# Kernel tuning notes

Hardware: AMD Instinct MI355X
Metric: run time of the kernel (lower is better)

The kernel has to match this reference:

```python
import jax, jax.numpy as jnp
import numpy as np

D_MODEL = 1024
D_CTRL = 1024
N_HEADS = 16
TOPK = 4
TEMPERATURE = 1.0
LN_EPS = 1e-5


def layer_norm(x, g, b):
    m = jnp.mean(x, axis=-1, keepdims=True)
    v = jnp.mean(jnp.square(x - m), axis=-1, keepdims=True)
    return (x - m) * jax.lax.rsqrt(v + LN_EPS) * g + b


def setup_inputs() -> dict:
    key = jax.random.key(0)
    ks = jax.random.split(key, 8)
    B, S = 8, 2048
    s = 0.02
    return {
        "x": jax.random.normal(ks[0], (B, S, D_MODEL), dtype=jnp.float32),
        "state": jnp.zeros((B, D_CTRL), dtype=jnp.float32),
        # pool LayerNorm
        "pool_g": jnp.ones((D_MODEL,), jnp.float32),
        "pool_b": jnp.zeros((D_MODEL,), jnp.float32),
        # inp_proj
        "inp_w": jax.random.normal(ks[1], (D_MODEL, D_CTRL), jnp.float32) * s,
        "inp_b": jnp.zeros((D_CTRL,), jnp.float32),
        # W_z, W_h
        "wz_w": jax.random.normal(ks[2], (D_CTRL, D_CTRL), jnp.float32) * s,
        "wz_b": jnp.zeros((D_CTRL,), jnp.float32),
        "wh_w": jax.random.normal(ks[3], (D_CTRL, D_CTRL), jnp.float32) * s,
        "wh_b": jnp.zeros((D_CTRL,), jnp.float32),
        # ln_h
        "lnh_g": jnp.ones((D_CTRL,), jnp.float32),
        "lnh_b": jnp.zeros((D_CTRL,), jnp.float32),
        # router: LayerNorm(d_model+d_ctrl) -> Linear -> GELU -> Linear
        "rln_g": jnp.ones((D_MODEL + D_CTRL,), jnp.float32),
        "rln_b": jnp.zeros((D_MODEL + D_CTRL,), jnp.float32),
        "r_w1": jax.random.normal(ks[4], (D_MODEL + D_CTRL, D_CTRL), jnp.float32) * s,
        "r_b1": jnp.zeros((D_CTRL,), jnp.float32),
        "r_w2": jax.random.normal(ks[5], (D_CTRL, N_HEADS), jnp.float32) * s,
        "r_b2": jnp.zeros((N_HEADS,), jnp.float32),
    }


def reference(x, state, pool_g, pool_b, inp_w, inp_b, wz_w, wz_b, wh_w, wh_b,
              lnh_g, lnh_b, rln_g, rln_b, r_w1, r_b1, r_w2, r_b2):
    B, S, D = x.shape
    # pool: LayerNorm over tokens then mean over sequence -> [B, d_model]
    g = jnp.mean(layer_norm(x, pool_g, pool_b), axis=1)
    x_ctrl = g @ inp_w + inp_b  # [B, d_ctrl]
    z = jax.nn.sigmoid(x_ctrl @ wz_w + wz_b)
    h_cand = jnp.tanh(x_ctrl @ wh_w + wh_b)
    h_new = (1.0 - z) * state + z * h_cand
    h_new = layer_norm(h_new, lnh_g, lnh_b)  # [B, d_ctrl]
    # token-conditioned router on concat([X, h_tok])
    h_tok = jnp.broadcast_to(h_new[:, None, :], (B, S, D_CTRL))
    cat = jnp.concatenate([x, h_tok], axis=-1)  # [B, S, d_model+d_ctrl]
    hid = jax.nn.gelu(layer_norm(cat, rln_g, rln_b) @ r_w1 + r_b1, approximate=False)
    logits = hid @ r_w2 + r_b2  # [B, S, H]
    alpha = jax.nn.softmax(logits / TEMPERATURE, axis=-1)
    # top-k mask + renorm
    _, topi = jax.lax.top_k(alpha, TOPK)  # [B, S, k]
    mask = jnp.sum(jax.nn.one_hot(topi, N_HEADS, dtype=alpha.dtype), axis=-2)  # [B, S, H]
    masked = alpha * mask
    denom = jnp.maximum(jnp.sum(masked, axis=-1, keepdims=True), 1e-12)
    alpha = masked / denom
    entropy = -jnp.mean(jnp.sum(alpha * jnp.log(jnp.maximum(alpha, 1e-12)), axis=-1))
    return (alpha, h_new, entropy)
```

## Files before the change

### kernel.cpp

```cpp
#include <hip/hip_runtime.h>
#include <hip/hip_bf16.h>
#include <math.h>

typedef unsigned short u16;
typedef __attribute__((ext_vector_type(8))) short bf16x8;
typedef __attribute__((ext_vector_type(4))) float f32x4;
typedef __attribute__((ext_vector_type(4))) unsigned short u16x4;

#define B_ 8
#define S_ 2048
#define T_ 16384
#define D_ 1024
#define H_ 16
#define EPS_ 1e-5f

__device__ __forceinline__ u16 f2bf(float f) {
    __hip_bfloat16 h = __float2bfloat16(f);
    union { __hip_bfloat16 h; u16 u; } cv; cv.h = h; return cv.u;
}
__device__ __forceinline__ float bf2f(u16 u) {
    union { u16 u; __hip_bfloat16 h; } cv; cv.u = u; return __bfloat162float(cv.h);
}

__global__ __launch_bounds__(256) void k0a(const float* __restrict__ rw1,
        const float* __restrict__ rlng, const float* __restrict__ rlnb,
        u16* __restrict__ whiT, u16* __restrict__ wloT,
        float* __restrict__ c1part, float* __restrict__ c2part) {
    int nb = blockIdx.x, kb = blockIdx.y;
    int t = threadIdx.x;
    int nl = t & 63, kq = t >> 6;
    int n0 = nb * 64, k0 = kb * 64;
    __shared__ float ld[64][65];
    __shared__ float red[2][4][64];
    float a1 = 0.f, a2 = 0.f;
    #pragma unroll
    for (int r = 0; r < 16; ++r) {
        int kl = r * 4 + kq;
        int k = k0 + kl, n = n0 + nl;
        float w0 = rw1[(size_t)k * 1024 + n];
        ld[kl][nl] = w0;
        a1 += rlng[k] * w0;
        a2 += rlnb[k] * w0;
    }
    red[0][kq][nl] = a1;
    red[1][kq][nl] = a2;
    __syncthreads();
    if (t < 64) {
        c1part[(size_t)kb * 1024 + n0 + t] = red[0][0][t] + red[0][1][t] + red[0][2][t] + red[0][3][t];
        c2part[(size_t)kb * 1024 + n0 + t] = red[1][0][t] + red[1][1][t] + red[1][2][t] + red[1][3][t];
    }
    if (kb < 16) {
        #pragma unroll
        for (int r = 0; r < 16; ++r) {
            int nl2 = r * 4 + kq;
            int k = k0 + nl, n = n0 + nl2;
            float w0 = ld[nl][nl2] * rlng[k];
            u16 hi = f2bf(w0);
            float lo = w0 - bf2f(hi);
            whiT[(size_t)n * 1024 + k] = hi;
            wloT[(size_t)n * 1024 + k] = f2bf(lo);
        }
    }
}

__global__ __launch_bounds__(256) void k1(const float* __restrict__ x,
        u16* __restrict__ xhi, u16* __restrict__ xlo,
        float* __restrict__ sx, float* __restrict__ sxx, float* __restrict__ gpart) {
    int blk = blockIdx.x;
    int b = blk >> 5, chunk = blk & 31;
    int tid = threadIdx.x, w = tid >> 6, lane = tid & 63;
    __shared__ float lacc[4][1024];
    float acc[4][4];
    #pragma unroll
    for (int j = 0; j < 4; ++j)
        #pragma unroll
        for (int c = 0; c < 4; ++c) acc[j][c] = 0.f;

    for (int i = 0; i < 16; ++i) {
        int s = chunk * 64 + i * 4 + w;
        size_t tok = (size_t)b * S_ + s;
        size_t base = tok * D_;
        float4 v[4];
        float sum = 0.f, ssq = 0.f;
        #pragma unroll
        for (int j = 0; j < 4; ++j) {
            v[j] = *(const float4*)&x[base + j * 256 + lane * 4];
            sum += v[j].x + v[j].y + v[j].z + v[j].w;
            ssq += v[j].x * v[j].x + v[j].y * v[j].y + v[j].z * v[j].z + v[j].w * v[j].w;
        }
        #pragma unroll
        for (int m = 1; m < 64; m <<= 1) { sum += __shfl_xor(sum, m); ssq += __shfl_xor(ssq, m); }
        float mean = sum * (1.f / 1024.f);
        float var = ssq * (1.f / 1024.f) - mean * mean;
        float rstd = rsqrtf(var + EPS_);
        if (lane == 0) { sx[tok] = sum; sxx[tok] = ssq; }
        #pragma unroll
        for (int j = 0; j < 4; ++j) {
            float xs[4] = { v[j].x, v[j].y, v[j].z, v[j].w };
            u16 hs[4], ls[4];
            #pragma unroll
            for (int c = 0; c < 4; ++c) {
                acc[j][c] += (xs[c] - mean) * rstd;
                u16 h = f2bf(xs[c]);
                hs[c] = h;
                ls[c] = f2bf(xs[c] - bf2f(h));
            }
            size_t o = base + j * 256 + lane * 4;
            *(u16x4*)&xhi[o] = (u16x4){ hs[0], hs[1], hs[2], hs[3] };
            *(u16x4*)&xlo[o] = (u16x4){ ls[0], ls[1], ls[2], ls[3] };
        }
    }
    #pragma unroll
    for (int j = 0; j < 4; ++j)
        #pragma unroll
        for (int c = 0; c < 4; ++c) lacc[w][j * 256 + lane * 4 + c] = acc[j][c];
    __syncthreads();
    for (int q = 0; q < 4; ++q) {
        int n = q * 256 + tid;
        gpart[((size_t)b * 32 + chunk) * 1024 + n] =
            lacc[0][n] + lacc[1][n] + lacc[2][n] + lacc[3][n];
    }
}

__global__ __launch_bounds__(256) void kgemv_g(const float* __restrict__ gpart,
        const float* __restrict__ pg, const float* __restrict__ pb,
        const float* __restrict__ W, float* __restrict__ part) {
    int t = threadIdx.x;
    int n = blockIdx.x * 256 + t;
    int k0 = blockIdx.y * 32;
    __shared__ float sg[8][32];
    {
        int b = t >> 5, k = t & 31;
        float s = 0.f;
        #pragma unroll 8
        for (int p = 0; p < 32; ++p) s += gpart[((size_t)b * 32 + p) * 1024 + k0 + k];
        sg[b][k] = s * (1.f / 2048.f) * pg[k0 + k] + pb[k0 + k];
    }
    __syncthreads();
    float acc[8] = {};
    #pragma unroll
    for (int k = 0; k < 32; ++k) {
        float wv = W[(size_t)(k0 + k) * 1024 + n];
        #pragma unroll
        for (int b = 0; b < 8; ++b) acc[b] += sg[b][k] * wv;
    }
    #pragma unroll
    for (int b = 0; b < 8; ++b)
        part[((size_t)blockIdx.y * 8 + b) * 1024 + n] = acc[b];
}

__global__ __launch_bounds__(256) void kgemv_split(const float* __restrict__ in,
        const float* __restrict__ W, const float* __restrict__ scale,
        float* __restrict__ part) {
    int t = threadIdx.x;
    int n = blockIdx.x * 256 + t;
    int k0 = blockIdx.y * 32;
    __shared__ float sg[8][32];
    {
        int b = t >> 5, k = t & 31;
        float v = in[b * 1024 + k0 + k];
        if (scale) v *= scale[k0 + k];
        sg[b][k] = v;
    }
    __syncthreads();
    float acc[8] = {};
    #pragma unroll
    for (int k = 0; k < 32; ++k) {
        float wv = W[(size_t)(k0 + k) * 1024 + n];
        #pragma unroll
        for (int b = 0; b < 8; ++b) acc[b] += sg[b][k] * wv;
    }
    #pragma unroll
    for (int b = 0; b < 8; ++b)
        part[((size_t)blockIdx.y * 8 + b) * 1024 + n] = acc[b];
}

__global__ __launch_bounds__(256) void kgemv2_f(const float* __restrict__ partIn,
        const float* __restrict__ bias,
        const float* __restrict__ Wz, const float* __restrict__ Wh,
        float* __restrict__ zpart, float* __restrict__ hpart) {
    int t = threadIdx.x;
    int n = blockIdx.x * 256 + t;
    int k0 = blockIdx.y * 32;
    __shared__ float sg[8][32];
    {
        int b = t >> 5, k = t & 31;
        float s = bias[k0 + k];
        #pragma unroll 8
        for (int p = 0; p < 32; ++p) s += partIn[((size_t)p * 8 + b) * 1024 + k0 + k];
        sg[b][k] = s;
    }
    __syncthreads();
    float az[8] = {}, ah[8] = {};
    #pragma unroll
    for (int k = 0; k < 32; ++k) {
        size_t o = (size_t)(k0 + k) * 1024 + n;
        float wz = Wz[o];
        float wh = Wh[o];
        #pragma unroll
        for (int b = 0; b < 8; ++b) { az[b] += sg[b][k] * wz; ah[b] += sg[b][k] * wh; }
    }
    #pragma unroll
    for (int b = 0; b < 8; ++b) {
        size_t o = ((size_t)blockIdx.y * 8 + b) * 1024 + n;
        zpart[o] = az[b];
        hpart[o] = ah[b];
    }
}

__global__ __launch_bounds__(256) void k3b_red_ln(const float* __restrict__ zpart,
        const float* __restrict__ hpart, const float* __restrict__ bz,
        const float* __restrict__ bh, const float* __restrict__ state,
        const float* __restrict__ lg, const float* __restrict__ lb,
        float* __restrict__ hnew, float* __restrict__ outh,
        float* __restrict__ shb, float* __restrict__ shhb) {
    int b = blockIdx.x, tid = threadIdx.x;
    int w = tid >> 6, lane = tid & 63;
    __shared__ float rbuf[4][2];
    float hp[4];
    float sum = 0.f, ssq = 0.f;
    #pragma unroll
    for (int q = 0; q < 4; ++q) {
        int n = q * 256 + tid;
        float az = bz[n], ah = bh[n];
        #pragma unroll 8
        for (int p = 0; p < 32; ++p) {
            size_t o = ((size_t)p * 8 + b) * 1024 + n;
            az += zpart[o];
            ah += hpart[o];
        }
        float z = 1.f / (1.f + expf(-az));
        float hc = tanhf(ah);
        float v = (1.f - z) * state[(size_t)b * 1024 + n] + z * hc;
        hp[q] = v; sum += v; ssq += v * v;
    }
    #pragma unroll
    for (int m = 1; m < 64; m <<= 1) { sum += __shfl_xor(sum, m); ssq += __shfl_xor(ssq, m); }
    if (lane == 0) { rbuf[w][0] = sum; rbuf[w][1] = ssq; }
    __syncthreads();
    sum = rbuf[0][0] + rbuf[1][0] + rbuf[2][0] + rbuf[3][0];
    ssq = rbuf[0][1] + rbuf[1][1] + rbuf[2][1] + rbuf[3][1];
    float mean = sum * (1.f / 1024.f);
    float var = ssq * (1.f / 1024.f) - mean * mean;
    float rstd = rsqrtf(var + EPS_);
    float s2 = 0.f, q2 = 0.f;
    #pragma unroll
    for (int q = 0; q < 4; ++q) {
        int n = q * 256 + tid;
        float h = (hp[q] - mean) * rstd * lg[n] + lb[n];
        hnew[(size_t)b * 1024 + n] = h;
        outh[(size_t)b * 1024 + n] = h;
        s2 += h; q2 += h * h;
    }
    #pragma unroll
    for (int m = 1; m < 64; m <<= 1) { s2 += __shfl_xor(s2, m); q2 += __shfl_xor(q2, m); }
    __syncthreads();
    if (lane == 0) { rbuf[w][0] = s2; rbuf[w][1] = q2; }
    __syncthreads();
    if (tid == 0) {
        shb[b] = rbuf[0][0] + rbuf[1][0] + rbuf[2][0] + rbuf[3][0];
        shhb[b] = rbuf[0][1] + rbuf[1][1] + rbuf[2][1] + rbuf[3][1];
    }
}

__global__ __launch_bounds__(256) void kprep(const float* __restrict__ vpartIn,
        const float* __restrict__ c1part, const float* __restrict__ c2part,
        const float* __restrict__ rb1,
        const float* __restrict__ sx, const float* __restrict__ sxx,
        const float* __restrict__ shb, const float* __restrict__ shhb,
        float* __restrict__ vmat, float* __restrict__ c1, float* __restrict__ dvec,
        float* __restrict__ pt, float* __restrict__ qt) {
    int blk = blockIdx.x, tid = threadIdx.x;
    if (blk < 32) {
        int i = blk * 256 + tid;
        int b = i >> 10, n = i & 1023;
        float s = 0.f;
        #pragma unroll 8
        for (int p = 0; p < 32; ++p) s += vpartIn[((size_t)p * 8 + b) * 1024 + n];
        vmat[i] = s;
    } else if (blk < 36) {
        int n = (blk - 32) * 256 + tid;
        float s1 = 0.f, s2 = 0.f;
        for (int p = 0; p < 32; ++p) { s1 += c1part[p * 1024 + n]; s2 += c2part[p * 1024 + n]; }
        c1[n] = s1;
        dvec[n] = s2 + rb1[n];
    } else {
        int t = (blk - 36) * 256 + tid;
        int b = t >> 11;
        float m = (sx[t] + shb[b]) * (1.f / 2048.f);
        float var = (sxx[t] + shhb[b]) * (1.f / 2048.f) - m * m;
        float rstd = rsqrtf(var + EPS_);
        pt[t] = rstd;
        qt[t] = -m * rstd;
    }
}

__device__ __forceinline__ void gl16(const void* g, void* l) {
    __builtin_amdgcn_global_load_lds((const __attribute__((address_space(1))) void*)g,
                                     (__attribute__((address_space(3))) void*)l, 16, 0, 0);
}

__global__ __launch_bounds__(256, 1) void k5_gemm(
        const u16* __restrict__ xhi, const u16* __restrict__ xlo,
        const u16* __restrict__ whiT, const u16* __restrict__ wloT,
        const float* __restrict__ pt, const float* __restrict__ qt,
        const float* __restrict__ vmat, const float* __restrict__ c1,
        const float* __restrict__ dvec, const float* __restrict__ rw2,
        float* __restrict__ lpart) {
    __shared__ unsigned char smem[66048];
    u16* sAh = (u16*)smem;
    u16* sAl = sAh + 128 * 64;
    u16* sBh = sAl + 128 * 64;
    u16* sBl = sBh + 128 * 64;
    float* shid = (float*)smem;

    int bid = blockIdx.x;
    int x8 = bid & 7, j = bid >> 3;
    int mb = x8 * 16 + (j >> 3);
    int nb = j & 7;
    int tid = threadIdx.x;
    int lane = tid & 63, wid = tid >> 6;
    int wm = wid >> 1, wn = wid & 1;
    int l16 = lane & 15, lq = lane >> 4;

    f32x4 acc[4][4] = {};

    size_t aBase = (size_t)mb * 128 * 1024;
    size_t bBase = (size_t)nb * 128 * 1024;

    for (int kb = 0; kb < 16; ++kb) {
        __syncthreads();
        #pragma unroll
        for (int i = 0; i < 4; ++i) {
            int chunk = tid + 256 * i;
            int row = chunk >> 3, c8 = chunk & 7;
            int s8 = c8 ^ (row & 7);
            size_t go = (size_t)row * 1024 + (size_t)kb * 64 + s8 * 8;
            int lo = chunk * 16;
            gl16(xhi + aBase + go, (char*)sAh + lo);
            gl16(xlo + aBase + go, (char*)sAl + lo);
            gl16(whiT + bBase + go, (char*)sBh + lo);
            gl16(wloT + bBase + go, (char*)sBl + lo);
        }
        asm volatile("s_waitcnt vmcnt(0)" ::: "memory");
        __syncthreads();
        #pragma unroll
        for (int kk = 0; kk < 2; ++kk) {
            bf16x8 ah[4], al[4], bh[4], bl[4];
            int sl = ((kk * 4 + lq) ^ (l16 & 7)) * 8;
            #pragma unroll
            for (int f = 0; f < 4; ++f) {
                int ar = wm * 64 + f * 16 + l16;
                int br = wn * 64 + f * 16 + l16;
                ah[f] = *(const bf16x8*)&sAh[ar * 64 + sl];
                al[f] = *(const bf16x8*)&sAl[ar * 64 + sl];
                bh[f] = *(const bf16x8*)&sBh[br * 64 + sl];
                bl[f] = *(const bf16x8*)&sBl[br * 64 + sl];
            }
            #pragma unroll
            for (int mf = 0; mf < 4; ++mf)
                #pragma unroll
                for (int nf = 0; nf < 4; ++nf) {
                    acc[mf][nf] = __builtin_amdgcn_mfma_f32_16x16x32_bf16(ah[mf], bh[nf], acc[mf][nf], 0, 0, 0);
                    acc[mf][nf] = __builtin_amdgcn_mfma_f32_16x16x32_bf16(ah[mf], bl[nf], acc[mf][nf], 0, 0, 0);
                    acc[mf][nf] = __builtin_amdgcn_mfma_f32_16x16x32_bf16(al[mf], bh[nf], acc[mf][nf], 0, 0, 0);
                }
        }
    }
    __syncthreads();

    int token0 = mb * 128;
    int bidx = token0 >> 11;
    const float* vrow = vmat + (size_t)bidx * 1024;
    float vn[4], c1n[4], dn[4];
    #pragma unroll
    for (int nf = 0; nf < 4; ++nf) {
        int n = nb * 128 + wn * 64 + nf * 16 + l16;
        vn[nf] = vrow[n]; c1n[nf] = c1[n]; dn[nf] = dvec[n];
    }
    #pragma unroll
    for (int mf = 0; mf < 4; ++mf) {
        #pragma unroll
        for (int r = 0; r < 4; ++r) {
            int rowl = wm * 64 + mf * 16 + lq * 4 + r;
            float p = pt[token0 + rowl];
            float q = qt[token0 + rowl];
            #pragma unroll
            for (int nf = 0; nf < 4; ++nf) {
                int coll = wn * 64 + nf * 16 + l16;
                float pre = p * (acc[mf][nf][r] + vn[nf]) + q * c1n[nf] + dn[nf];
                float hid = 0.5f * pre * (1.f + erff(pre * 0.70710678118f));
                shid[rowl * 129 + coll] = hid;
            }
        }
    }
    __syncthreads();

    int r2 = tid >> 1, half = tid & 1;
    const float* w2b = rw2 + (size_t)nb * 128 * 16 + half * 8;
    float a8[8];
    #pragma unroll
    for (int h = 0; h < 8; ++h) a8[h] = 0.f;
    #pragma unroll 8
    for (int j2 = 0; j2 < 128; ++j2) {
        float hv = shid[r2 * 129 + j2];
        float4 w0 = *(const float4*)(w2b + (size_t)j2 * 16);
        float4 w1 = *(const float4*)(w2b + (size_t)j2 * 16 + 4);
        a8[0] += hv * w0.x; a8[1] += hv * w0.y; a8[2] += hv * w0.z; a8[3] += hv * w0.w;
        a8[4] += hv * w1.x; a8[5] += hv * w1.y; a8[6] += hv * w1.z; a8[7] += hv * w1.w;
    }
    float* lp = lpart + ((size_t)nb * T_ + token0 + r2) * 16 + half * 8;
    #pragma unroll
    for (int h = 0; h < 8; ++h) lp[h] = a8[h];
}

__global__ __launch_bounds__(256) void k6(const float* __restrict__ lpart,
        const float* __restrict__ rb2, float* __restrict__ alpha_out,
        float* __restrict__ entpart) {
    int blk = blockIdx.x;
    int tid = threadIdx.x;
    int token = blk * 16 + (tid >> 4);
    int h = tid & 15;
    float lg = rb2[h];
    #pragma unroll
    for (int p = 0; p < 8; ++p) lg += lpart[((size_t)p * T_ + token) * 16 + h];

    float mx = lg;
    #pragma unroll
    for (int m = 1; m < 16; m <<= 1) mx = fmaxf(mx, __shfl_xor(mx, m));
    float e = expf(lg - mx);
    float sum = e;
    #pragma unroll
    for (int m = 1; m < 16; m <<= 1) sum += __shfl_xor(sum, m);
    float a0 = e / sum;

    float work = lg;
    bool sel = false;
    #pragma unroll
    for (int it = 0; it < 4; ++it) {
        float bv = work; int bi = h;
        #pragma unroll
        for (int m = 1; m < 16; m <<= 1) {
            float ov = __shfl_xor(bv, m); int oi = __shfl_xor(bi, m);
            if (ov > bv || (ov == bv && oi < bi)) { bv = ov; bi = oi; }
        }
        if (h == bi) { sel = true; work = -1e30f; }
    }
    float am = sel ? a0 : 0.f;
    float den = am;
    #pragma unroll
    for (int m = 1; m < 16; m <<= 1) den += __shfl_xor(den, m);
    den = fmaxf(den, 1e-12f);
    float a = am / den;
    alpha_out[(size_t)token * 16 + h] = a;

    float term = a * logf(fmaxf(a, 1e-12f));
    #pragma unroll
    for (int m = 1; m < 64; m <<= 1) term += __shfl_xor(term, m);
    __shared__ float tw[4];
    if ((tid & 63) == 0) tw[tid >> 6] = term;
    __syncthreads();
    if (tid == 0) entpart[blk] = tw[0] + tw[1] + tw[2] + tw[3];
}

__global__ __launch_bounds__(256) void k7(const float* __restrict__ entpart,
        float* __restrict__ out_ent) {
    int tid = threadIdx.x;
    float s = 0.f;
    for (int i = tid; i < 1024; i += 256) s += entpart[i];
    #pragma unroll
    for (int m = 1; m < 64; m <<= 1) s += __shfl_xor(s, m);
    __shared__ float tw[4];
    if ((tid & 63) == 0) tw[tid >> 6] = s;
    __syncthreads();
    if (tid == 0) out_ent[0] = -(tw[0] + tw[1] + tw[2] + tw[3]) * (1.f / (float)T_);
}

extern "C" void kernel_launch(void* const* d_in, const int* in_sizes, int n_in,
                              void* d_out, int out_size, void* d_ws, size_t ws_size,
                              hipStream_t stream) {
    const float* x     = (const float*)d_in[0];
    const float* state = (const float*)d_in[1];
    const float* pg    = (const float*)d_in[2];
    const float* pbv   = (const float*)d_in[3];
    const float* inpw  = (const float*)d_in[4];
    const float* inpb  = (const float*)d_in[5];
    const float* wzw   = (const float*)d_in[6];
    const float* wzb   = (const float*)d_in[7];
    const float* whw   = (const float*)d_in[8];
    const float* whb   = (const float*)d_in[9];
    const float* lnhg  = (const float*)d_in[10];
    const float* lnhb  = (const float*)d_in[11];
    const float* rlng  = (const float*)d_in[12];
    const float* rlnb  = (const float*)d_in[13];
    const float* rw1   = (const float*)d_in[14];
    const float* rb1   = (const float*)d_in[15];
    const float* rw2   = (const float*)d_in[16];
    const float* rb2   = (const float*)d_in[17];
    float* out = (float*)d_out;
    (void)in_sizes; (void)n_in; (void)out_size; (void)ws_size;

    char* base = (char*)d_ws;
    size_t off = 0;
    auto alloc = [&](size_t bytes) -> char* {
        char* p = base + off;
        off = (off + bytes + 255) & ~(size_t)255;
        return p;
    };
    u16*   xhi    = (u16*)alloc((size_t)T_ * D_ * 2);
    u16*   xlo    = (u16*)alloc((size_t)T_ * D_ * 2);
    u16*   whiT   = (u16*)alloc((size_t)D_ * D_ * 2);
    u16*   wloT   = (u16*)alloc((size_t)D_ * D_ * 2);
    float* c1part = (float*)alloc(32 * 1024 * 4);
    float* c2part = (float*)alloc(32 * 1024 * 4);
    float* c1     = (float*)alloc(1024 * 4);
    float* dvec   = (float*)alloc(1024 * 4);
    float* sx     = (float*)alloc((size_t)T_ * 4);
    float* sxx    = (float*)alloc((size_t)T_ * 4);
    float* ptv    = (float*)alloc((size_t)T_ * 4);
    float* qtv    = (float*)alloc((size_t)T_ * 4);
    float* gpart  = (float*)alloc((size_t)8 * 32 * 1024 * 4);
    float* hnew   = (float*)alloc(8 * 1024 * 4);
    float* vmat   = (float*)alloc(8 * 1024 * 4);
    float* shb    = (float*)alloc(256);
    float* shhb   = (float*)alloc(256);
    float* lpart  = (float*)alloc((size_t)8 * T_ * H_ * 4);
    float* entpart= (float*)alloc(1024 * 4);
    float* partA  = (float*)alloc((size_t)32 * 8 * 1024 * 4);
    float* partB  = (float*)alloc((size_t)32 * 8 * 1024 * 4);
    float* partC  = (float*)alloc((size_t)32 * 8 * 1024 * 4);

    k0a<<<dim3(16, 32), 256, 0, stream>>>(rw1, rlng, rlnb, whiT, wloT, c1part, c2part);
    k1<<<256, 256, 0, stream>>>(x, xhi, xlo, sx, sxx, gpart);
    kgemv_g<<<dim3(4, 32), 256, 0, stream>>>(gpart, pg, pbv, inpw, partA);
    kgemv2_f<<<dim3(4, 32), 256, 0, stream>>>(partA, inpb, wzw, whw, partB, partC);
    k3b_red_ln<<<8, 256, 0, stream>>>(partB, partC, wzb, whb, state, lnhg, lnhb,
                                      hnew, out + (size_t)T_ * H_, shb, shhb);
    kgemv_split<<<dim3(4, 32), 256, 0, stream>>>(hnew, rw1 + (size_t)1024 * 1024,
                                                 rlng + 1024, partA);
    kprep<<<100, 256, 0, stream>>>(partA, c1part, c2part, rb1, sx, sxx, shb, shhb,
                                   vmat, c1, dvec, ptv, qtv);
    k5_gemm<<<1024, 256, 0, stream>>>(xhi, xlo, whiT, wloT, ptv, qtv, vmat,
                                      c1, dvec, rw2, lpart);
    k6<<<1024, 256, 0, stream>>>(lpart, rb2, out, entpart);
    k7<<<1, 256, 0, stream>>>(entpart, out + (size_t)T_ * H_ + (size_t)B_ * D_);
}
```

Before: 203.0 us.

## Merge prep kernels and read GEMM B tiles directly from global memory

Merges the weight-prep and x-split kernels into one launch, folds the c1/dvec reduction into the first GEMV kernel, and moves the token-stat computation into the hnew GEMV kernel, splitting the vmat reduction into its own small kernel. In the main GEMM, the B operand (whiT/wloT) is no longer staged in LDS and is loaded per fragment straight from global memory. LDS use drops by half, and the epilogue processes the hidden tile in two 64-row halves. The aim is fewer launches and higher occupancy, at the cost of uncached, redundant global loads for B, which may be slower.

New measurement: 270.2 us. 1.33x slower.

```diff
diff --git a/kernel.cpp b/kernel.cpp
--- a/kernel.cpp
+++ b/kernel.cpp
@@ -22,157 +22,142 @@
     union { u16 u; __hip_bfloat16 h; } cv; cv.u = u; return __bfloat162float(cv.h);
 }
 
-__global__ __launch_bounds__(256) void k0a(const float* __restrict__ rw1,
-        const float* __restrict__ rlng, const float* __restrict__ rlnb,
-        u16* __restrict__ whiT, u16* __restrict__ wloT,
+__global__ __launch_bounds__(256) void k01(const float* __restrict__ x,
+        u16* __restrict__ xhi, u16* __restrict__ xlo,
+        float* __restrict__ sx, float* __restrict__ sxx, float* __restrict__ gpart,
+        const float* __restrict__ rw1, const float* __restrict__ rlng,
+        const float* __restrict__ rlnb, u16* __restrict__ whiT, u16* __restrict__ wloT,
         float* __restrict__ c1part, float* __restrict__ c2part) {
-    int nb = blockIdx.x, kb = blockIdx.y;
-    int t = threadIdx.x;
-    int nl = t & 63, kq = t >> 6;
-    int n0 = nb * 64, k0 = kb * 64;
+    __shared__ float lacc[4][1024];
     __shared__ float ld[64][65];
     __shared__ float red[2][4][64];
-    float a1 = 0.f, a2 = 0.f;
-    #pragma unroll
-    for (int r = 0; r < 16; ++r) {
-        int kl = r * 4 + kq;
-        int k = k0 + kl, n = n0 + nl;
-        float w0 = rw1[(size_t)k * 1024 + n];
-        ld[kl][nl] = w0;
-        a1 += rlng[k] * w0;
-        a2 += rlnb[k] * w0;
-    }
-    red[0][kq][nl] = a1;
-    red[1][kq][nl] = a2;
-    __syncthreads();
-    if (t < 64) {
-        c1part[(size_t)kb * 1024 + n0 + t] = red[0][0][t] + red[0][1][t] + red[0][2][t] + red[0][3][t];
-        c2part[(size_t)kb * 1024 + n0 + t] = red[1][0][t] + red[1][1][t] + red[1][2][t] + red[1][3][t];
-    }
-    if (kb < 16) {
+    int blk = blockIdx.x;
+    int tid = threadIdx.x;
+    if (blk < 256) {
+        int b = blk >> 5, chunk = blk & 31;
+        int w = tid >> 6, lane = tid & 63;
+        float acc[4][4];
+        #pragma unroll
+        for (int j = 0; j < 4; ++j)
+            #pragma unroll
+            for (int c = 0; c < 4; ++c) acc[j][c] = 0.f;
+        for (int i = 0; i < 16; ++i) {
+            int s = chunk * 64 + i * 4 + w;
+            size_t tok = (size_t)b * S_ + s;
+            size_t base = tok * D_;
+            float4 v[4];
+            float sum = 0.f, ssq = 0.f;
+            #pragma unroll
+            for (int j = 0; j < 4; ++j) {
+                v[j] = *(const float4*)&x[base + j * 256 + lane * 4];
+                sum += v[j].x + v[j].y + v[j].z + v[j].w;
+                ssq += v[j].x * v[j].x + v[j].y * v[j].y + v[j].z * v[j].z + v[j].w * v[j].w;
+            }
+            #pragma unroll
+            for (int m = 1; m < 64; m <<= 1) { sum += __shfl_xor(sum, m); ssq += __shfl_xor(ssq, m); }
+            float mean = sum * (1.f / 1024.f);
+            float var = ssq * (1.f / 1024.f) - mean * mean;
+            float rstd = rsqrtf(var + EPS_);
+            if (lane == 0) { sx[tok] = sum; sxx[tok] = ssq; }
+            #pragma unroll
+            for (int j = 0; j < 4; ++j) {
+                float xs[4] = { v[j].x, v[j].y, v[j].z, v[j].w };
+                u16 hs[4], ls[4];
+                #pragma unroll
+                for (int c = 0; c < 4; ++c) {
+                    acc[j][c] += (xs[c] - mean) * rstd;
+                    u16 h = f2bf(xs[c]);
+                    hs[c] = h;
+                    ls[c] = f2bf(xs[c] - bf2f(h));
+                }
+                size_t o = base + j * 256 + lane * 4;
+                *(u16x4*)&xhi[o] = (u16x4){ hs[0], hs[1], hs[2], hs[3] };
+                *(u16x4*)&xlo[o] = (u16x4){ ls[0], ls[1], ls[2], ls[3] };
+            }
+        }
+        #pragma unroll
+        for (int j = 0; j < 4; ++j)
+            #pragma unroll
+            for (int c = 0; c < 4; ++c) lacc[w][j * 256 + lane * 4 + c] = acc[j][c];
+        __syncthreads();
+        for (int q = 0; q < 4; ++q) {
+            int n = q * 256 + tid;
+            gpart[((size_t)b * 32 + chunk) * 1024 + n] =
+                lacc[0][n] + lacc[1][n] + lacc[2][n] + lacc[3][n];
+        }
+    } else {
+        int idx = blk - 256;
+        int nb = idx & 15, kb = idx >> 4;
+        int nl = tid & 63, kq = tid >> 6;
+        int n0 = nb * 64, k0 = kb * 64;
+        float a1 = 0.f, a2 = 0.f;
         #pragma unroll
         for (int r = 0; r < 16; ++r) {
-            int nl2 = r * 4 + kq;
-            int k = k0 + nl, n = n0 + nl2;
-            float w0 = ld[nl][nl2] * rlng[k];
-            u16 hi = f2bf(w0);
-            float lo = w0 - bf2f(hi);
-            whiT[(size_t)n * 1024 + k] = hi;
-            wloT[(size_t)n * 1024 + k] = f2bf(lo);
-        }
-    }
-}
-
-__global__ __launch_bounds__(256) void k1(const float* __restrict__ x,
-        u16* __restrict__ xhi, u16* __restrict__ xlo,
-        float* __restrict__ sx, float* __restrict__ sxx, float* __restrict__ gpart) {
-    int blk = blockIdx.x;
-    int b = blk >> 5, chunk = blk & 31;
-    int tid = threadIdx.x, w = tid >> 6, lane = tid & 63;
-    __shared__ float lacc[4][1024];
-    float acc[4][4];
-    #pragma unroll
-    for (int j = 0; j < 4; ++j)
-        #pragma unroll
-        for (int c = 0; c < 4; ++c) acc[j][c] = 0.f;
-
-    for (int i = 0; i < 16; ++i) {
-        int s = chunk * 64 + i * 4 + w;
-        size_t tok = (size_t)b * S_ + s;
-        size_t base = tok * D_;
-        float4 v[4];
-        float sum = 0.f, ssq = 0.f;
-        #pragma unroll
-        for (int j = 0; j < 4; ++j) {
-            v[j] = *(const float4*)&x[base + j * 256 + lane * 4];
-            sum += v[j].x + v[j].y + v[j].z + v[j].w;
-            ssq += v[j].x * v[j].x + v[j].y * v[j].y + v[j].z * v[j].z + v[j].w * v[j].w;
-        }
-        #pragma unroll
-        for (int m = 1; m < 64; m <<= 1) { sum += __shfl_xor(sum, m); ssq += __shfl_xor(ssq, m); }
-        float mean = sum * (1.f / 1024.f);
-        float var = ssq * (1.f / 1024.f) - mean * mean;
-        float rstd = rsqrtf(var + EPS_);
-        if (lane == 0) { sx[tok] = sum; sxx[tok] = ssq; }
-        #pragma unroll
-        for (int j = 0; j < 4; ++j) {
-            float xs[4] = { v[j].x, v[j].y, v[j].z, v[j].w };
-            u16 hs[4], ls[4];
-            #pragma unroll
-            for (int c = 0; c < 4; ++c) {
-                acc[j][c] += (xs[c] - mean) * rstd;
-                u16 h = f2bf(xs[c]);
-                hs[c] = h;
-                ls[c] = f2bf(xs[c] - bf2f(h));
+            int kl = r * 4 + kq;
+            int k = k0 + kl, n = n0 + nl;
+            float w0 = rw1[(size_t)k * 1024 + n];
+            ld[kl][nl] = w0;
+            a1 += rlng[k] * w0;
+            a2 += rlnb[k] * w0;
+        }
+        red[0][kq][nl] = a1;
+        red[1][kq][nl] = a2;
+        __syncthreads();
+        if (tid < 64) {
+            c1part[(size_t)kb * 1024 + n0 + tid] = red[0][0][tid] + red[0][1][tid] + red[0][2][tid] + red[0][3][tid];
+            c2part[(size_t)kb * 1024 + n0 + tid] = red[1][0][tid] + red[1][1][tid] + red[1][2][tid] + red[1][3][tid];
+        }
+        if (kb < 16) {
+            #pragma unroll
+            for (int r = 0; r < 16; ++r) {
+                int nl2 = r * 4 + kq;
+                int k = k0 + nl, n = n0 + nl2;
+                float w0 = ld[nl][nl2] * rlng[k];
+                u16 hi = f2bf(w0);
+                float lo = w0 - bf2f(hi);
+                whiT[(size_t)n * 1024 + k] = hi;
+                wloT[(size_t)n * 1024 + k] = f2bf(lo);
             }
-            size_t o = base + j * 256 + lane * 4;
-            *(u16x4*)&xhi[o] = (u16x4){ hs[0], hs[1], hs[2], hs[3] };
-            *(u16x4*)&xlo[o] = (u16x4){ ls[0], ls[1], ls[2], ls[3] };
-        }
-    }
-    #pragma unroll
-    for (int j = 0; j < 4; ++j)
-        #pragma unroll
-        for (int c = 0; c < 4; ++c) lacc[w][j * 256 + lane * 4 + c] = acc[j][c];
-    __syncthreads();
-    for (int q = 0; q < 4; ++q) {
-        int n = q * 256 + tid;
-        gpart[((size_t)b * 32 + chunk) * 1024 + n] =
-            lacc[0][n] + lacc[1][n] + lacc[2][n] + lacc[3][n];
-    }
-}
-
-__global__ __launch_bounds__(256) void kgemv_g(const float* __restrict__ gpart,
+        }
+    }
+}
+
+__global__ __launch_bounds__(256) void kB(const float* __restrict__ gpart,
         const float* __restrict__ pg, const float* __restrict__ pb,
-        const float* __restrict__ W, float* __restrict__ part) {
-    int t = threadIdx.x;
-    int n = blockIdx.x * 256 + t;
-    int k0 = blockIdx.y * 32;
-    __shared__ float sg[8][32];
-    {
-        int b = t >> 5, k = t & 31;
-        float s = 0.f;
-        #pragma unroll 8
-        for (int p = 0; p < 32; ++p) s += gpart[((size_t)b * 32 + p) * 1024 + k0 + k];
-        sg[b][k] = s * (1.f / 2048.f) * pg[k0 + k] + pb[k0 + k];
-    }
-    __syncthreads();
-    float acc[8] = {};
-    #pragma unroll
-    for (int k = 0; k < 32; ++k) {
-        float wv = W[(size_t)(k0 + k) * 1024 + n];
-        #pragma unroll
-        for (int b = 0; b < 8; ++b) acc[b] += sg[b][k] * wv;
-    }
-    #pragma unroll
-    for (int b = 0; b < 8; ++b)
-        part[((size_t)blockIdx.y * 8 + b) * 1024 + n] = acc[b];
-}
-
-__global__ __launch_bounds__(256) void kgemv_split(const float* __restrict__ in,
-        const float* __restrict__ W, const float* __restrict__ scale,
-        float* __restrict__ part) {
-    int t = threadIdx.x;
-    int n = blockIdx.x * 256 + t;
-    int k0 = blockIdx.y * 32;
-    __shared__ float sg[8][32];
-    {
-        int b = t >> 5, k = t & 31;
-        float v = in[b * 1024 + k0 + k];
-        if (scale) v *= scale[k0 + k];
-        sg[b][k] = v;
-    }
-    __syncthreads();
-    float acc[8] = {};
-    #pragma unroll
-    for (int k = 0; k < 32; ++k) {
-        float wv = W[(size_t)(k0 + k) * 1024 + n];
-        #pragma unroll
-        for (int b = 0; b < 8; ++b) acc[b] += sg[b][k] * wv;
-    }
-    #pragma unroll
-    for (int b = 0; b < 8; ++b)
-        part[((size_t)blockIdx.y * 8 + b) * 1024 + n] = acc[b];
+        const float* __restrict__ W, float* __restrict__ part,
+        const float* __restrict__ c1part, const float* __restrict__ c2part,
+        const float* __restrict__ rb1, float* __restrict__ c1, float* __restrict__ dvec) {
+    int blk = blockIdx.x, t = threadIdx.x;
+    if (blk < 128) {
+        int nBlk = blk & 3, ks = blk >> 2;
+        int n = nBlk * 256 + t;
+        int k0 = ks * 32;
+        __shared__ float sg[8][32];
+        {
+            int b = t >> 5, k = t & 31;
+            float s = 0.f;
+            #pragma unroll 8
+            for (int p = 0; p < 32; ++p) s += gpart[((size_t)b * 32 + p) * 1024 + k0 + k];
+            sg[b][k] = s * (1.f / 2048.f) * pg[k0 + k] + pb[k0 + k];
+        }
+        __syncthreads();
+        float acc[8] = {};
+        #pragma unroll
+        for (int k = 0; k < 32; ++k) {
+            float wv = W[(size_t)(k0 + k) * 1024 + n];
+            #pragma unroll
+            for (int b = 0; b < 8; ++b) acc[b] += sg[b][k] * wv;
+        }
+        #pragma unroll
+        for (int b = 0; b < 8; ++b)
+            part[((size_t)ks * 8 + b) * 1024 + n] = acc[b];
+    } else {
+        int n = (blk - 128) * 256 + t;
+        float s1 = 0.f, s2 = 0.f;
+        for (int p = 0; p < 32; ++p) { s1 += c1part[p * 1024 + n]; s2 += c2part[p * 1024 + n]; }
+        c1[n] = s1;
+        dvec[n] = s2 + rb1[n];
+    }
 }
 
 __global__ __launch_bounds__(256) void kgemv2_f(const float* __restrict__ partIn,
@@ -263,36 +248,52 @@
     }
 }
 
-__global__ __launch_bounds__(256) void kprep(const float* __restrict__ vpartIn,
-        const float* __restrict__ c1part, const float* __restrict__ c2part,
-        const float* __restrict__ rb1,
+__global__ __launch_bounds__(256) void kE(const float* __restrict__ in,
+        const float* __restrict__ W, const float* __restrict__ scale,
+        float* __restrict__ part,
         const float* __restrict__ sx, const float* __restrict__ sxx,
         const float* __restrict__ shb, const float* __restrict__ shhb,
-        float* __restrict__ vmat, float* __restrict__ c1, float* __restrict__ dvec,
         float* __restrict__ pt, float* __restrict__ qt) {
-    int blk = blockIdx.x, tid = threadIdx.x;
-    if (blk < 32) {
-        int i = blk * 256 + tid;
-        int b = i >> 10, n = i & 1023;
-        float s = 0.f;
-        #pragma unroll 8
-        for (int p = 0; p < 32; ++p) s += vpartIn[((size_t)p * 8 + b) * 1024 + n];
-        vmat[i] = s;
-    } else if (blk < 36) {
-        int n = (blk - 32) * 256 + tid;
-        float s1 = 0.f, s2 = 0.f;
-        for (int p = 0; p < 32; ++p) { s1 += c1part[p * 1024 + n]; s2 += c2part[p * 1024 + n]; }
-        c1[n] = s1;
-        dvec[n] = s2 + rb1[n];
+    int blk = blockIdx.x, t = threadIdx.x;
+    if (blk < 128) {
+        int nBlk = blk & 3, ks = blk >> 2;
+        int n = nBlk * 256 + t;
+        int k0 = ks * 32;
+        __shared__ float sg[8][32];
+        {
+            int b = t >> 5, k = t & 31;
+            sg[b][k] = in[b * 1024 + k0 + k] * scale[k0 + k];
+        }
+        __syncthreads();
+        float acc[8] = {};
+        #pragma unroll
+        for (int k = 0; k < 32; ++k) {
+            float wv = W[(size_t)(k0 + k) * 1024 + n];
+            #pragma unroll
+            for (int b = 0; b < 8; ++b) acc[b] += sg[b][k] * wv;
+        }
+        #pragma unroll
+        for (int b = 0; b < 8; ++b)
+            part[((size_t)ks * 8 + b) * 1024 + n] = acc[b];
     } else {
-        int t = (blk - 36) * 256 + tid;
-        int b = t >> 11;
-        float m = (sx[t] + shb[b]) * (1.f / 2048.f);
-        float var = (sxx[t] + shhb[b]) * (1.f / 2048.f) - m * m;
+        int tok = (blk - 128) * 256 + t;
+        int b = tok >> 11;
+        float m = (sx[tok] + shb[b]) * (1.f / 2048.f);
+        float var = (sxx[tok] + shhb[b]) * (1.f / 2048.f) - m * m;
         float rstd = rsqrtf(var + EPS_);
-        pt[t] = rstd;
-        qt[t] = -m * rstd;
-    }
+        pt[tok] = rstd;
+        qt[tok] = -m * rstd;
+    }
+}
+
+__global__ __launch_bounds__(256) void kF(const float* __restrict__ part,
+        float* __restrict__ vmat) {
+    int i = blockIdx.x * 256 + threadIdx.x;
+    int b = i >> 10, n = i & 1023;
+    float s = 0.f;
+    #pragma unroll 8
+    for (int p = 0; p < 32; ++p) s += part[((size_t)p * 8 + b) * 1024 + n];
+    vmat[i] = s;
 }
 
 __device__ __forceinline__ void gl16(const void* g, void* l) {
@@ -307,11 +308,9 @@
         const float* __restrict__ vmat, const float* __restrict__ c1,
         const float* __restrict__ dvec, const float* __restrict__ rw2,
         float* __restrict__ lpart) {
-    __shared__ unsigned char smem[66048];
+    __shared__ unsigned char smem[33024];
     u16* sAh = (u16*)smem;
     u16* sAl = sAh + 128 * 64;
-    u16* sBh = sAl + 128 * 64;
-    u16* sBl = sBh + 128 * 64;
     float* shid = (float*)smem;
 
     int bid = blockIdx.x;
@@ -336,11 +335,8 @@
             int row = chunk >> 3, c8 = chunk & 7;
             int s8 = c8 ^ (row & 7);
             size_t go = (size_t)row * 1024 + (size_t)kb * 64 + s8 * 8;
-            int lo = chunk * 16;
-            gl16(xhi + aBase + go, (char*)sAh + lo);
-            gl16(xlo + aBase + go, (char*)sAl + lo);
-            gl16(whiT + bBase + go, (char*)sBh + lo);
-            gl16(wloT + bBase + go, (char*)sBl + lo);
+            gl16(xhi + aBase + go, (char*)sAh + chunk * 16);
+            gl16(xlo + aBase + go, (char*)sAl + chunk * 16);
         }
         asm volatile("s_waitcnt vmcnt(0)" ::: "memory");
         __syncthreads();
@@ -352,10 +348,11 @@
             for (int f = 0; f < 4; ++f) {
                 int ar = wm * 64 + f * 16 + l16;
                 int br = wn * 64 + f * 16 + l16;
+                size_t gb = bBase + (size_t)br * 1024 + (size_t)kb * 64 + kk * 32 + lq * 8;
                 ah[f] = *(const bf16x8*)&sAh[ar * 64 + sl];
                 al[f] = *(const bf16x8*)&sAl[ar * 64 + sl];
-                bh[f] = *(const bf16x8*)&sBh[br * 64 + sl];
-                bl[f] = *(const bf16x8*)&sBl[br * 64 + sl];
+                bh[f] = *(const bf16x8*)&whiT[gb];
+                bl[f] = *(const bf16x8*)&wloT[gb];
             }
             #pragma unroll
             for (int mf = 0; mf < 4; ++mf)
@@ -367,7 +364,6 @@
                 }
         }
     }
-    __syncthreads();
 
     int token0 = mb * 128;
     int bidx = token0 >> 11;
@@ -379,39 +375,39 @@
         vn[nf] = vrow[n]; c1n[nf] = c1[n]; dn[nf] = dvec[n];
     }
     #pragma unroll
-    for (int mf = 0; mf < 4; ++mf) {
-        #pragma unroll
-        for (int r = 0; r < 4; ++r) {
-            int rowl = wm * 64 + mf * 16 + lq * 4 + r;
-            float p = pt[token0 + rowl];
-            float q = qt[token0 + rowl];
-            #pragma unroll
-            for (int nf = 0; nf < 4; ++nf) {
-                int coll = wn * 64 + nf * 16 + l16;
-                float pre = p * (acc[mf][nf][r] + vn[nf]) + q * c1n[nf] + dn[nf];
-                float hid = 0.5f * pre * (1.f + erff(pre * 0.70710678118f));
-                shid[rowl * 129 + coll] = hid;
+    for (int c = 0; c < 2; ++c) {
+        __syncthreads();
+        if (wm == c) {
+            #pragma unroll
+            for (int mf = 0; mf < 4; ++mf) {
+                #pragma unroll
+                for (int r = 0; r < 4; ++r) {
+                    int rloc = mf * 16 + lq * 4 + r;
+                    int tok = token0 + c * 64 + rloc;
+                    float p = pt[tok];
+                    float q = qt[tok];
+                    #pragma unroll
+                    for (int nf = 0; nf < 4; ++nf) {
+                        int coll = wn * 64 + nf * 16 + l16;
+                        float pre = p * (acc[mf][nf][r] + vn[nf]) + q * c1n[nf] + dn[nf];
+                        shid[rloc * 129 + coll] = 0.5f * pre * (1.f + erff(pre * 0.70710678118f));
+                    }
+                }
             }
         }
-    }
-    __syncthreads();
-
-    int r2 = tid >> 1, half = tid & 1;
-    const float* w2b = rw2 + (size_t)nb * 128 * 16 + half * 8;
-    float a8[8];
-    #pragma unroll
-    for (int h = 0; h < 8; ++h) a8[h] = 0.f;
-    #pragma unroll 8
-    for (int j2 = 0; j2 < 128; ++j2) {
-        float hv = shid[r2 * 129 + j2];
-        float4 w0 = *(const float4*)(w2b + (size_t)j2 * 16);
-        float4 w1 = *(const float4*)(w2b + (size_t)j2 * 16 + 4);
-        a8[0] += hv * w0.x; a8[1] += hv * w0.y; a8[2] += hv * w0.z; a8[3] += hv * w0.w;
-        a8[4] += hv * w1.x; a8[5] += hv * w1.y; a8[6] += hv * w1.z; a8[7] += hv * w1.w;
-    }
-    float* lp = lpart + ((size_t)nb * T_ + token0 + r2) * 16 + half * 8;
-    #pragma unroll
-    for (int h = 0; h < 8; ++h) lp[h] = a8[h];
+        __syncthreads();
+        int rloc = tid >> 2, q4 = tid & 3;
+        const float* w2b = rw2 + (size_t)nb * 128 * 16 + q4 * 4;
+        float a4[4] = {};
+        #pragma unroll 8
+        for (int jj = 0; jj < 128; ++jj) {
+            float hv = shid[rloc * 129 + jj];
+            float4 w = *(const float4*)(w2b + (size_t)jj * 16);
+            a4[0] += hv * w.x; a4[1] += hv * w.y; a4[2] += hv * w.z; a4[3] += hv * w.w;
+        }
+        float* lp = lpart + ((size_t)nb * T_ + token0 + c * 64 + rloc) * 16 + q4 * 4;
+        lp[0] = a4[0]; lp[1] = a4[1]; lp[2] = a4[2]; lp[3] = a4[3];
+    }
 }
 
 __global__ __launch_bounds__(256) void k6(const float* __restrict__ lpart,
@@ -530,16 +526,16 @@
     float* partB  = (float*)alloc((size_t)32 * 8 * 1024 * 4);
     float* partC  = (float*)alloc((size_t)32 * 8 * 1024 * 4);
 
-    k0a<<<dim3(16, 32), 256, 0, stream>>>(rw1, rlng, rlnb, whiT, wloT, c1part, c2part);
-    k1<<<256, 256, 0, stream>>>(x, xhi, xlo, sx, sxx, gpart);
-    kgemv_g<<<dim3(4, 32), 256, 0, stream>>>(gpart, pg, pbv, inpw, partA);
+    k01<<<768, 256, 0, stream>>>(x, xhi, xlo, sx, sxx, gpart,
+                                 rw1, rlng, rlnb, whiT, wloT, c1part, c2part);
+    kB<<<132, 256, 0, stream>>>(gpart, pg, pbv, inpw, partA,
+                                c1part, c2part, rb1, c1, dvec);
     kgemv2_f<<<dim3(4, 32), 256, 0, stream>>>(partA, inpb, wzw, whw, partB, partC);
     k3b_red_ln<<<8, 256, 0, stream>>>(partB, partC, wzb, whb, state, lnhg, lnhb,
                                       hnew, out + (size_t)T_ * H_, shb, shhb);
-    kgemv_split<<<dim3(4, 32), 256, 0, stream>>>(hnew, rw1 + (size_t)1024 * 1024,
-                                                 rlng + 1024, partA);
-    kprep<<<100, 256, 0, stream>>>(partA, c1part, c2part, rb1, sx, sxx, shb, shhb,
-                                   vmat, c1, dvec, ptv, qtv);
+    kE<<<192, 256, 0, stream>>>(hnew, rw1 + (size_t)1024 * 1024, rlng + 1024, partA,
+                                sx, sxx, shb, shhb, ptv, qtv);
+    kF<<<32, 256, 0, stream>>>(partA, vmat);
     k5_gemm<<<1024, 256, 0, stream>>>(xhi, xlo, whiT, wloT, ptv, qtv, vmat,
                                       c1, dvec, rw2, lpart);
     k6<<<1024, 256, 0, stream>>>(lpart, rb2, out, entpart);
```
